# Kernel optimization log

Hardware: AMD Instinct MI355X
Metric: run time of the kernel (lower is better)

## Reference

```python
import jax, jax.numpy as jnp
import numpy as np

E = 8        # n_experts
H = 1024     # hidden_size == input_size
M = 2048     # intermediate_size
K = 2        # topk
SE = 1       # share_expert
BSZ, SEQ = 2, 1024
W_SCALE = 0.02


def setup_inputs() -> dict:
    key = jax.random.key(0)
    ks = jax.random.split(key, 9)
    return {
        "x": jax.random.normal(ks[0], (BSZ, SEQ, H), jnp.float32),
        "gate_w": jax.random.normal(ks[1], (E, H), jnp.float32) * W_SCALE,
        "beta": jnp.zeros((E,), jnp.float32),
        "gate_proj_w": jax.random.normal(ks[2], (E, H, M), jnp.float32) * W_SCALE,
        "up_proj_w": jax.random.normal(ks[3], (E, H, M), jnp.float32) * W_SCALE,
        "down_proj_w": jax.random.normal(ks[4], (E, M, H), jnp.float32) * W_SCALE,
        "shared_gate_w": jax.random.normal(ks[5], (SE, H, M), jnp.float32) * W_SCALE,
        "shared_up_w": jax.random.normal(ks[6], (SE, H, M), jnp.float32) * W_SCALE,
        "shared_down_w": jax.random.normal(ks[7], (SE, M, H), jnp.float32) * W_SCALE,
    }


def reference(x, gate_w, beta, gate_proj_w, up_proj_w, down_proj_w,
              shared_gate_w, shared_up_w, shared_down_w):
    B0, S0, H0 = x.shape
    xt = x.reshape(-1, H0)                       # [B, H], B = B0*S0 tokens
    B = xt.shape[0]

    # --- routing: top-k on (logits + beta), gate prob = sigmoid(selected logits) ---
    logits = xt @ gate_w.T                       # [B, E]
    _, idx = jax.lax.top_k(logits + beta, K)     # [B, K] expert indices
    probs = jax.nn.sigmoid(jnp.take_along_axis(logits, idx, axis=-1))  # [B, K]

    # combine weights c[b, e]: scatter top-k probs (equivalent to index_add combine)
    c = jnp.zeros((B, E), xt.dtype).at[jnp.arange(B)[:, None], idx].add(probs)

    # --- per-expert SwiGLU over all tokens, then weighted combine by c ---
    g = jnp.einsum('bh,ehm->bem', xt, gate_proj_w)   # [B, E, M]
    u = jnp.einsum('bh,ehm->bem', xt, up_proj_w)     # [B, E, M]
    h = jax.nn.silu(g) * u                           # [B, E, M]
    eo = jnp.einsum('bem,emh->beh', h, down_proj_w)  # [B, E, H]
    combined = jnp.einsum('beh,be->bh', eo, c)       # [B, H]

    # --- shared expert(s): applied to every token, no gating ---
    sg = jnp.einsum('bh,ehm->bem', xt, shared_gate_w)
    su = jnp.einsum('bh,ehm->bem', xt, shared_up_w)
    sh = jax.nn.silu(sg) * su
    shared_out = jnp.einsum('bem,emh->beh', sh, shared_down_w).sum(axis=1)  # [B, H]

    return (combined + shared_out).reshape(B0, S0, H0)
```

## Files before the change

### kernel.cpp

```cpp
#include <hip/hip_runtime.h>

#define NE 8
#define HD 1024
#define MD 2048
#define NT 2048
#define NSH 4096

typedef __attribute__((ext_vector_type(8))) short s16x8;
typedef __attribute__((ext_vector_type(4))) float f32x4;
typedef __attribute__((ext_vector_type(4))) unsigned short u16x4;
typedef __attribute__((ext_vector_type(2))) unsigned short u16x2;

__device__ __forceinline__ unsigned short f2bf(float f) {
    union { float f; unsigned int i; } v; v.f = f;
    unsigned int u = v.i;
    return (unsigned short)((u + 0x7FFFu + ((u >> 16) & 1u)) >> 16);
}
__device__ __forceinline__ float bf2f(unsigned short u) {
    union { unsigned int i; float f; } v; v.i = ((unsigned int)u) << 16; return v.f;
}

__device__ __forceinline__ void gld16(const unsigned short* g, short* l) {
    __builtin_amdgcn_global_load_lds(
        (const __attribute__((address_space(1))) unsigned int*)g,
        (__attribute__((address_space(3))) unsigned int*)l,
        16, 0, 0);
}

__global__ __launch_bounds__(256) void k_cvt(
    const float* __restrict__ s, unsigned short* __restrict__ d, int n)
{
    int i = (blockIdx.x * 256 + threadIdx.x) * 4;
    int stride = gridDim.x * 256 * 4;
    for (; i < n; i += stride) {
        float4 v = *(const float4*)(s + i);
        u16x4 o;
        o[0] = f2bf(v.x); o[1] = f2bf(v.y); o[2] = f2bf(v.z); o[3] = f2bf(v.w);
        *(u16x4*)(d + i) = o;
    }
}

__global__ __launch_bounds__(1024) void k_cvt_t(
    const float* __restrict__ wr, const float* __restrict__ wsd,
    unsigned short* __restrict__ o, int K, int N)
{
    int e = blockIdx.z;
    const float* src = (e < NE) ? wr + (size_t)e * K * N : wsd;
    unsigned short* dst = o + (size_t)e * N * K;
    int k0 = blockIdx.x * 64, n0 = blockIdx.y * 32;
    __shared__ float T[64 * 33];
    int tx = threadIdx.x, ty = threadIdx.y;
    T[(2 * ty) * 33 + tx]     = src[(size_t)(k0 + 2 * ty) * N + n0 + tx];
    T[(2 * ty + 1) * 33 + tx] = src[(size_t)(k0 + 2 * ty + 1) * N + n0 + tx];
    __syncthreads();
    float a = T[(2 * tx) * 33 + ty];
    float b = T[(2 * tx + 1) * 33 + ty];
    u16x2 r; r[0] = f2bf(a); r[1] = f2bf(b);
    *(u16x2*)(dst + (size_t)(n0 + ty) * K + k0 + 2 * tx) = r;
}

__global__ __launch_bounds__(256) void k_route(
    const float* __restrict__ x, const float* __restrict__ gw,
    const float* __restrict__ beta,
    int* __restrict__ cnt, int* __restrict__ list, int* __restrict__ slot,
    float* __restrict__ rprob)
{
    int wave = threadIdx.x >> 6, lane = threadIdx.x & 63;
    int t = blockIdx.x * 4 + wave;
    const float4* xp = (const float4*)(x + (size_t)t * HD) + lane * 4;
    float4 xv[4];
    #pragma unroll
    for (int j = 0; j < 4; j++) xv[j] = xp[j];

    float logit[NE];
    #pragma unroll
    for (int e = 0; e < NE; e++) {
        const float4* gp = (const float4*)(gw + e * HD) + lane * 4;
        float s = 0.f;
        #pragma unroll
        for (int j = 0; j < 4; j++) {
            float4 g = gp[j];
            s += xv[j].x * g.x + xv[j].y * g.y + xv[j].z * g.z + xv[j].w * g.w;
        }
        for (int off = 32; off > 0; off >>= 1) s += __shfl_xor(s, off);
        logit[e] = s;
    }
    if (lane == 0) {
        float v[NE];
        #pragma unroll
        for (int e = 0; e < NE; e++) v[e] = logit[e] + beta[e];
        int i1 = 0; float m1 = v[0];
        #pragma unroll
        for (int e = 1; e < NE; e++) if (v[e] > m1) { m1 = v[e]; i1 = e; }
        int i2 = -1; float m2 = -3.4e38f;
        #pragma unroll
        for (int e = 0; e < NE; e++) if (e != i1 && v[e] > m2) { m2 = v[e]; i2 = e; }
        if (i2 < 0) i2 = (i1 + 1) & 7;
        float p1 = 1.f / (1.f + __expf(-logit[i1]));
        float p2 = 1.f / (1.f + __expf(-logit[i2]));
        int pos1 = atomicAdd(cnt + i1, 1);
        list[i1 * NT + pos1] = t; slot[t * 2 + 0] = (i1 << 16) | pos1; rprob[t * 2 + 0] = p1;
        int pos2 = atomicAdd(cnt + i2, 1);
        list[i2 * NT + pos2] = t; slot[t * 2 + 1] = (i2 << 16) | pos2; rprob[t * 2 + 1] = p2;
    }
}

__global__ void k_scan(const int* __restrict__ cnt, int* __restrict__ base) {
    if (threadIdx.x == 0) {
        int run = 0;
        for (int e = 0; e < NE; e++) { base[e] = run; run += cnt[e]; }
        base[NE] = run;
    }
}

__global__ __launch_bounds__(256) void k_gateup(
    const unsigned short* __restrict__ x,
    const unsigned short* __restrict__ wg_all, const unsigned short* __restrict__ wu_all,
    const int* __restrict__ cnt, const int* __restrict__ base, const int* __restrict__ list,
    unsigned short* __restrict__ h)
{
    int e = blockIdx.z;
    int i0 = blockIdx.y * 128;
    int n0 = blockIdx.x * 128;
    int cnte = (e < NE) ? cnt[e] : NT;
    if (i0 >= cnte) return;
    int rbase = (e < NE) ? base[e] : NSH;
    const unsigned short* wg = wg_all + (size_t)e * HD * MD;
    const unsigned short* wu = wu_all + (size_t)e * HD * MD;

    __shared__ short As[128 * 32];
    __shared__ short Bg[128 * 32];
    __shared__ short Bu[128 * 32];
    __shared__ int tok[128];

    int tid = threadIdx.x;
    int lane = tid & 63, wave = tid >> 6;
    if (tid < 128) {
        int gi = i0 + tid;
        tok[tid] = (e < NE) ? ((gi < cnte) ? list[e * NT + gi] : list[e * NT]) : gi;
    }
    __syncthreads();

    int rr = wave * 32 + (lane >> 2);
    int kc = (lane & 3) * 8;
    size_t gaA0 = (size_t)tok[rr] * HD + kc;
    size_t gaA1 = (size_t)tok[rr + 16] * HD + kc;
    size_t gaB0 = (size_t)(n0 + rr) * HD + kc;
    size_t gaB1 = (size_t)(n0 + rr + 16) * HD + kc;
    short* lA0 = &As[(wave * 32) * 32];
    short* lA1 = &As[(wave * 32 + 16) * 32];
    short* lB0 = &Bg[(wave * 32) * 32];
    short* lB1 = &Bg[(wave * 32 + 16) * 32];
    short* lU0 = &Bu[(wave * 32) * 32];
    short* lU1 = &Bu[(wave * 32 + 16) * 32];

    int wr = (wave >> 1) * 64, wc = (wave & 1) * 64;
    int m = lane & 15, q = lane >> 4;

    f32x4 accG[4][4], accU[4][4];
    #pragma unroll
    for (int a = 0; a < 4; a++)
        #pragma unroll
        for (int b = 0; b < 4; b++) { accG[a][b] = (f32x4)0.f; accU[a][b] = (f32x4)0.f; }

    for (int k0 = 0; k0 < HD; k0 += 32) {
        __syncthreads();
        gld16(x + gaA0 + k0, lA0);
        gld16(x + gaA1 + k0, lA1);
        gld16(wg + gaB0 + k0, lB0);
        gld16(wg + gaB1 + k0, lB1);
        gld16(wu + gaB0 + k0, lU0);
        gld16(wu + gaB1 + k0, lU1);
        __syncthreads();

        s16x8 af[4];
        #pragma unroll
        for (int ti = 0; ti < 4; ti++)
            af[ti] = *(const s16x8*)(&As[(wr + ti * 16 + m) * 32 + q * 8]);
        #pragma unroll
        for (int tj = 0; tj < 4; tj++) {
            int nn = wc + tj * 16 + m;
            s16x8 bg = *(const s16x8*)(&Bg[nn * 32 + q * 8]);
            s16x8 bu = *(const s16x8*)(&Bu[nn * 32 + q * 8]);
            #pragma unroll
            for (int ti = 0; ti < 4; ti++) {
                accG[ti][tj] = __builtin_amdgcn_mfma_f32_16x16x32_bf16(af[ti], bg, accG[ti][tj], 0, 0, 0);
                accU[ti][tj] = __builtin_amdgcn_mfma_f32_16x16x32_bf16(af[ti], bu, accU[ti][tj], 0, 0, 0);
            }
        }
    }
    #pragma unroll
    for (int ti = 0; ti < 4; ti++)
        #pragma unroll
        for (int tj = 0; tj < 4; tj++)
            #pragma unroll
            for (int r = 0; r < 4; r++) {
                int gi = i0 + wr + ti * 16 + q * 4 + r;
                if (gi < cnte) {
                    int col = n0 + wc + tj * 16 + m;
                    float g = accG[ti][tj][r], u = accU[ti][tj][r];
                    float hv = (g / (1.f + __expf(-g))) * u;
                    h[(size_t)(rbase + gi) * MD + col] = f2bf(hv);
                }
            }
}

__global__ __launch_bounds__(256) void k_down(
    const unsigned short* __restrict__ wd_all,
    const int* __restrict__ cnt, const int* __restrict__ base,
    const unsigned short* __restrict__ h, unsigned short* __restrict__ eo)
{
    int e = blockIdx.z;
    int i0 = blockIdx.y * 128;
    int n0 = blockIdx.x * 128;
    int cnte = (e < NE) ? cnt[e] : NT;
    if (i0 >= cnte) return;
    int rbase = (e < NE) ? base[e] : NSH;
    const unsigned short* wd = wd_all + (size_t)e * MD * HD;

    __shared__ short As[128 * 32];
    __shared__ short Bd[128 * 32];

    int tid = threadIdx.x;
    int lane = tid & 63, wave = tid >> 6;
    int rr = wave * 32 + (lane >> 2);
    int kc = (lane & 3) * 8;
    size_t gaA0 = (size_t)(rbase + i0 + rr) * MD + kc;
    size_t gaA1 = (size_t)(rbase + i0 + rr + 16) * MD + kc;
    size_t gaB0 = (size_t)(n0 + rr) * MD + kc;
    size_t gaB1 = (size_t)(n0 + rr + 16) * MD + kc;
    short* lA0 = &As[(wave * 32) * 32];
    short* lA1 = &As[(wave * 32 + 16) * 32];
    short* lB0 = &Bd[(wave * 32) * 32];
    short* lB1 = &Bd[(wave * 32 + 16) * 32];

    int wr = (wave >> 1) * 64, wc = (wave & 1) * 64;
    int m = lane & 15, q = lane >> 4;

    f32x4 acc[4][4];
    #pragma unroll
    for (int a = 0; a < 4; a++)
        #pragma unroll
        for (int b = 0; b < 4; b++) acc[a][b] = (f32x4)0.f;

    for (int k0 = 0; k0 < MD; k0 += 32) {
        __syncthreads();
        gld16(h + gaA0 + k0, lA0);
        gld16(h + gaA1 + k0, lA1);
        gld16(wd + gaB0 + k0, lB0);
        gld16(wd + gaB1 + k0, lB1);
        __syncthreads();

        s16x8 af[4];
        #pragma unroll
        for (int ti = 0; ti < 4; ti++)
            af[ti] = *(const s16x8*)(&As[(wr + ti * 16 + m) * 32 + q * 8]);
        #pragma unroll
        for (int tj = 0; tj < 4; tj++) {
            int nn = wc + tj * 16 + m;
            s16x8 bd = *(const s16x8*)(&Bd[nn * 32 + q * 8]);
            #pragma unroll
            for (int ti = 0; ti < 4; ti++)
                acc[ti][tj] = __builtin_amdgcn_mfma_f32_16x16x32_bf16(af[ti], bd, acc[ti][tj], 0, 0, 0);
        }
    }
    #pragma unroll
    for (int ti = 0; ti < 4; ti++)
        #pragma unroll
        for (int tj = 0; tj < 4; tj++)
            #pragma unroll
            for (int r = 0; r < 4; r++) {
                int gi = i0 + wr + ti * 16 + q * 4 + r;
                if (gi < cnte) {
                    int col = n0 + wc + tj * 16 + m;
                    eo[(size_t)(rbase + gi) * HD + col] = f2bf(acc[ti][tj][r]);
                }
            }
}

__global__ __launch_bounds__(256) void k_combine(
    const unsigned short* __restrict__ eo, const int* __restrict__ slot,
    const float* __restrict__ rprob, const int* __restrict__ base,
    float* __restrict__ out)
{
    int t = blockIdx.x;
    int s0 = slot[t * 2], s1 = slot[t * 2 + 1];
    float p0 = rprob[t * 2], p1 = rprob[t * 2 + 1];
    int r0 = base[s0 >> 16] + (s0 & 0xFFFF);
    int r1 = base[s1 >> 16] + (s1 & 0xFFFF);
    int rs = NSH + t;
    int c = threadIdx.x * 4;
    u16x4 a = *(const u16x4*)(eo + (size_t)r0 * HD + c);
    u16x4 b = *(const u16x4*)(eo + (size_t)r1 * HD + c);
    u16x4 s = *(const u16x4*)(eo + (size_t)rs * HD + c);
    float4 res;
    res.x = p0 * bf2f(a[0]) + p1 * bf2f(b[0]) + bf2f(s[0]);
    res.y = p0 * bf2f(a[1]) + p1 * bf2f(b[1]) + bf2f(s[1]);
    res.z = p0 * bf2f(a[2]) + p1 * bf2f(b[2]) + bf2f(s[2]);
    res.w = p0 * bf2f(a[3]) + p1 * bf2f(b[3]) + bf2f(s[3]);
    *(float4*)(out + (size_t)t * HD + c) = res;
}

extern "C" void kernel_launch(void* const* d_in, const int* in_sizes, int n_in,
                              void* d_out, int out_size, void* d_ws, size_t ws_size,
                              hipStream_t stream)
{
    const float* x    = (const float*)d_in[0];
    const float* gw   = (const float*)d_in[1];
    const float* beta = (const float*)d_in[2];
    const float* wg   = (const float*)d_in[3];
    const float* wu   = (const float*)d_in[4];
    const float* wd   = (const float*)d_in[5];
    const float* swg  = (const float*)d_in[6];
    const float* swu  = (const float*)d_in[7];
    const float* swd  = (const float*)d_in[8];
    float* out = (float*)d_out;

    char* ws = (char*)d_ws;
    const size_t MB = (size_t)1 << 20;
    int*   cnt   = (int*)(ws + 0);
    int*   basep = (int*)(ws + 64);
    int*   list  = (int*)(ws + 1024);
    int*   slot  = (int*)(ws + 1024 + 65536);
    float* rprob = (float*)(ws + 1024 + 65536 + 16384);
    unsigned short* xb  = (unsigned short*)(ws + 1 * MB);
    unsigned short* wgt = (unsigned short*)(ws + 8 * MB);
    unsigned short* wut = (unsigned short*)(ws + 46 * MB);
    unsigned short* wdt = (unsigned short*)(ws + 84 * MB);
    unsigned short* h   = (unsigned short*)(ws + 122 * MB);
    unsigned short* eo  = (unsigned short*)(ws + 146 * MB);

    hipMemsetAsync(ws, 0, 128, stream);

    const int NX = NT * HD;
    k_cvt<<<512, 256, 0, stream>>>(x, xb, NX);

    dim3 tb(32, 32);
    dim3 tgu(HD / 64, MD / 32, NE + 1);
    k_cvt_t<<<tgu, tb, 0, stream>>>(wg, swg, wgt, HD, MD);
    k_cvt_t<<<tgu, tb, 0, stream>>>(wu, swu, wut, HD, MD);
    dim3 td(MD / 64, HD / 32, NE + 1);
    k_cvt_t<<<td, tb, 0, stream>>>(wd, swd, wdt, MD, HD);

    k_route<<<NT / 4, 256, 0, stream>>>(x, gw, beta, cnt, list, slot, rprob);
    k_scan<<<1, 64, 0, stream>>>(cnt, basep);

    dim3 g3(MD / 128, NT / 128, NE + 1);
    k_gateup<<<g3, 256, 0, stream>>>(xb, wgt, wut, cnt, basep, list, h);

    dim3 g4(HD / 128, NT / 128, NE + 1);
    k_down<<<g4, 256, 0, stream>>>(wdt, cnt, basep, h, eo);

    k_combine<<<NT, 256, 0, stream>>>(eo, slot, rprob, basep, out);
}
```

Measured before the change: 511.6 us.

## Double-buffer LDS tiles in expert GEMMs and vectorize weight transpose-convert

The gate/up and down GEMM kernels now use two LDS buffers, prefetching the next K-slice with global_load_lds while computing the current one. This removes one barrier per iteration and is meant to hide global memory latency. The weight transpose-convert kernel is rewritten to 256-thread blocks with float4 loads and 16-byte bf16 stores, to improve bandwidth on the large fp32 weight conversion. The cost is double the LDS use per block, which may lower occupancy. The prefetch relies on the load completing before the barrier at the top of the next iteration, with no explicit vmcnt wait.

```diff
diff --git a/kernel.cpp b/kernel.cpp
--- a/kernel.cpp
+++ b/kernel.cpp
@@ -8,8 +8,8 @@
 
 typedef __attribute__((ext_vector_type(8))) short s16x8;
 typedef __attribute__((ext_vector_type(4))) float f32x4;
+typedef __attribute__((ext_vector_type(8))) unsigned short u16x8;
 typedef __attribute__((ext_vector_type(4))) unsigned short u16x4;
-typedef __attribute__((ext_vector_type(2))) unsigned short u16x2;
 
 __device__ __forceinline__ unsigned short f2bf(float f) {
     union { float f; unsigned int i; } v; v.f = f;
@@ -40,23 +40,34 @@
     }
 }
 
-__global__ __launch_bounds__(1024) void k_cvt_t(
+__global__ __launch_bounds__(256) void k_cvt_t(
     const float* __restrict__ wr, const float* __restrict__ wsd,
     unsigned short* __restrict__ o, int K, int N)
 {
     int e = blockIdx.z;
     const float* src = (e < NE) ? wr + (size_t)e * K * N : wsd;
     unsigned short* dst = o + (size_t)e * N * K;
-    int k0 = blockIdx.x * 64, n0 = blockIdx.y * 32;
-    __shared__ float T[64 * 33];
-    int tx = threadIdx.x, ty = threadIdx.y;
-    T[(2 * ty) * 33 + tx]     = src[(size_t)(k0 + 2 * ty) * N + n0 + tx];
-    T[(2 * ty + 1) * 33 + tx] = src[(size_t)(k0 + 2 * ty + 1) * N + n0 + tx];
+    int k0 = blockIdx.x * 32, n0 = blockIdx.y * 128;
+    __shared__ float T[32 * 132];
+    int tid = threadIdx.x;
+    #pragma unroll
+    for (int p = 0; p < 4; p++) {
+        int k = (tid >> 5) + p * 8;
+        int n4 = (tid & 31) * 4;
+        float4 v = *(const float4*)(src + (size_t)(k0 + k) * N + n0 + n4);
+        *(float4*)(&T[k * 132 + n4]) = v;
+    }
     __syncthreads();
-    float a = T[(2 * tx) * 33 + ty];
-    float b = T[(2 * tx + 1) * 33 + ty];
-    u16x2 r; r[0] = f2bf(a); r[1] = f2bf(b);
-    *(u16x2*)(dst + (size_t)(n0 + ty) * K + k0 + 2 * tx) = r;
+    #pragma unroll
+    for (int p = 0; p < 2; p++) {
+        int idx = tid + p * 256;
+        int n = idx >> 2;
+        int kq = (idx & 3) * 8;
+        u16x8 r;
+        #pragma unroll
+        for (int j = 0; j < 8; j++) r[j] = f2bf(T[(kq + j) * 132 + n]);
+        *(u16x8*)(dst + (size_t)(n0 + n) * K + k0 + kq) = r;
+    }
 }
 
 __global__ __launch_bounds__(256) void k_route(
@@ -128,9 +139,9 @@
     const unsigned short* wg = wg_all + (size_t)e * HD * MD;
     const unsigned short* wu = wu_all + (size_t)e * HD * MD;
 
-    __shared__ short As[128 * 32];
-    __shared__ short Bg[128 * 32];
-    __shared__ short Bu[128 * 32];
+    __shared__ short As[2][128 * 32];
+    __shared__ short Bg[2][128 * 32];
+    __shared__ short Bu[2][128 * 32];
     __shared__ int tok[128];
 
     int tid = threadIdx.x;
@@ -147,12 +158,7 @@
     size_t gaA1 = (size_t)tok[rr + 16] * HD + kc;
     size_t gaB0 = (size_t)(n0 + rr) * HD + kc;
     size_t gaB1 = (size_t)(n0 + rr + 16) * HD + kc;
-    short* lA0 = &As[(wave * 32) * 32];
-    short* lA1 = &As[(wave * 32 + 16) * 32];
-    short* lB0 = &Bg[(wave * 32) * 32];
-    short* lB1 = &Bg[(wave * 32 + 16) * 32];
-    short* lU0 = &Bu[(wave * 32) * 32];
-    short* lU1 = &Bu[(wave * 32 + 16) * 32];
+    int lo0 = (wave * 32) * 32, lo1 = (wave * 32 + 16) * 32;
 
     int wr = (wave >> 1) * 64, wc = (wave & 1) * 64;
     int m = lane & 15, q = lane >> 4;
@@ -163,25 +169,35 @@
         #pragma unroll
         for (int b = 0; b < 4; b++) { accG[a][b] = (f32x4)0.f; accU[a][b] = (f32x4)0.f; }
 
-    for (int k0 = 0; k0 < HD; k0 += 32) {
+    gld16(x + gaA0, &As[0][lo0]);
+    gld16(x + gaA1, &As[0][lo1]);
+    gld16(wg + gaB0, &Bg[0][lo0]);
+    gld16(wg + gaB1, &Bg[0][lo1]);
+    gld16(wu + gaB0, &Bu[0][lo0]);
+    gld16(wu + gaB1, &Bu[0][lo1]);
+
+    int it = 0;
+    for (int k0 = 0; k0 < HD; k0 += 32, it ^= 1) {
         __syncthreads();
-        gld16(x + gaA0 + k0, lA0);
-        gld16(x + gaA1 + k0, lA1);
-        gld16(wg + gaB0 + k0, lB0);
-        gld16(wg + gaB1 + k0, lB1);
-        gld16(wu + gaB0 + k0, lU0);
-        gld16(wu + gaB1 + k0, lU1);
-        __syncthreads();
-
+        int nk = k0 + 32;
+        if (nk < HD) {
+            int nb = it ^ 1;
+            gld16(x + gaA0 + nk, &As[nb][lo0]);
+            gld16(x + gaA1 + nk, &As[nb][lo1]);
+            gld16(wg + gaB0 + nk, &Bg[nb][lo0]);
+            gld16(wg + gaB1 + nk, &Bg[nb][lo1]);
+            gld16(wu + gaB0 + nk, &Bu[nb][lo0]);
+            gld16(wu + gaB1 + nk, &Bu[nb][lo1]);
+        }
         s16x8 af[4];
         #pragma unroll
         for (int ti = 0; ti < 4; ti++)
-            af[ti] = *(const s16x8*)(&As[(wr + ti * 16 + m) * 32 + q * 8]);
+            af[ti] = *(const s16x8*)(&As[it][(wr + ti * 16 + m) * 32 + q * 8]);
         #pragma unroll
         for (int tj = 0; tj < 4; tj++) {
             int nn = wc + tj * 16 + m;
-            s16x8 bg = *(const s16x8*)(&Bg[nn * 32 + q * 8]);
-            s16x8 bu = *(const s16x8*)(&Bu[nn * 32 + q * 8]);
+            s16x8 bg = *(const s16x8*)(&Bg[it][nn * 32 + q * 8]);
+            s16x8 bu = *(const s16x8*)(&Bu[it][nn * 32 + q * 8]);
             #pragma unroll
             for (int ti = 0; ti < 4; ti++) {
                 accG[ti][tj] = __builtin_amdgcn_mfma_f32_16x16x32_bf16(af[ti], bg, accG[ti][tj], 0, 0, 0);
@@ -218,8 +234,8 @@
     int rbase = (e < NE) ? base[e] : NSH;
     const unsigned short* wd = wd_all + (size_t)e * MD * HD;
 
-    __shared__ short As[128 * 32];
-    __shared__ short Bd[128 * 32];
+    __shared__ short As[2][128 * 32];
+    __shared__ short Bd[2][128 * 32];
 
     int tid = threadIdx.x;
     int lane = tid & 63, wave = tid >> 6;
@@ -229,10 +245,7 @@
     size_t gaA1 = (size_t)(rbase + i0 + rr + 16) * MD + kc;
     size_t gaB0 = (size_t)(n0 + rr) * MD + kc;
     size_t gaB1 = (size_t)(n0 + rr + 16) * MD + kc;
-    short* lA0 = &As[(wave * 32) * 32];
-    short* lA1 = &As[(wave * 32 + 16) * 32];
-    short* lB0 = &Bd[(wave * 32) * 32];
-    short* lB1 = &Bd[(wave * 32 + 16) * 32];
+    int lo0 = (wave * 32) * 32, lo1 = (wave * 32 + 16) * 32;
 
     int wr = (wave >> 1) * 64, wc = (wave & 1) * 64;
     int m = lane & 15, q = lane >> 4;
@@ -243,22 +256,30 @@
         #pragma unroll
         for (int b = 0; b < 4; b++) acc[a][b] = (f32x4)0.f;
 
-    for (int k0 = 0; k0 < MD; k0 += 32) {
+    gld16(h + gaA0, &As[0][lo0]);
+    gld16(h + gaA1, &As[0][lo1]);
+    gld16(wd + gaB0, &Bd[0][lo0]);
+    gld16(wd + gaB1, &Bd[0][lo1]);
+
+    int it = 0;
+    for (int k0 = 0; k0 < MD; k0 += 32, it ^= 1) {
         __syncthreads();
-        gld16(h + gaA0 + k0, lA0);
-        gld16(h + gaA1 + k0, lA1);
-        gld16(wd + gaB0 + k0, lB0);
-        gld16(wd + gaB1 + k0, lB1);
-        __syncthreads();
-
+        int nk = k0 + 32;
+        if (nk < MD) {
+            int nb = it ^ 1;
+            gld16(h + gaA0 + nk, &As[nb][lo0]);
+            gld16(h + gaA1 + nk, &As[nb][lo1]);
+            gld16(wd + gaB0 + nk, &Bd[nb][lo0]);
+            gld16(wd + gaB1 + nk, &Bd[nb][lo1]);
+        }
         s16x8 af[4];
         #pragma unroll
         for (int ti = 0; ti < 4; ti++)
-            af[ti] = *(const s16x8*)(&As[(wr + ti * 16 + m) * 32 + q * 8]);
+            af[ti] = *(const s16x8*)(&As[it][(wr + ti * 16 + m) * 32 + q * 8]);
         #pragma unroll
         for (int tj = 0; tj < 4; tj++) {
             int nn = wc + tj * 16 + m;
-            s16x8 bd = *(const s16x8*)(&Bd[nn * 32 + q * 8]);
+            s16x8 bd = *(const s16x8*)(&Bd[it][nn * 32 + q * 8]);
             #pragma unroll
             for (int ti = 0; ti < 4; ti++)
                 acc[ti][tj] = __builtin_amdgcn_mfma_f32_16x16x32_bf16(af[ti], bd, acc[ti][tj], 0, 0, 0);
@@ -335,12 +356,11 @@
     const int NX = NT * HD;
     k_cvt<<<512, 256, 0, stream>>>(x, xb, NX);
 
-    dim3 tb(32, 32);
-    dim3 tgu(HD / 64, MD / 32, NE + 1);
-    k_cvt_t<<<tgu, tb, 0, stream>>>(wg, swg, wgt, HD, MD);
-    k_cvt_t<<<tgu, tb, 0, stream>>>(wu, swu, wut, HD, MD);
-    dim3 td(MD / 64, HD / 32, NE + 1);
-    k_cvt_t<<<td, tb, 0, stream>>>(wd, swd, wdt, MD, HD);
+    dim3 tgu(HD / 32, MD / 128, NE + 1);
+    k_cvt_t<<<tgu, 256, 0, stream>>>(wg, swg, wgt, HD, MD);
+    k_cvt_t<<<tgu, 256, 0, stream>>>(wu, swu, wut, HD, MD);
+    dim3 td(MD / 32, HD / 128, NE + 1);
+    k_cvt_t<<<td, 256, 0, stream>>>(wd, swd, wdt, MD, HD);
 
     k_route<<<NT / 4, 256, 0, stream>>>(x, gw, beta, cnt, list, slot, rprob);
     k_scan<<<1, 64, 0, stream>>>(cnt, basep);
```

Measured after the change: 508.3 us. Within noise of the previous version (-0.6%).
